# Kernel optimization log

Measured on AMD Instinct MI355X. Metric: run time of the kernel, lower is better.

The kernel has to match this reference:

```python
import jax, jax.numpy as jnp
import numpy as np
from jax import lax

B, CIN, COUT, K, H, W = 16, 256, 256, 3, 128, 128
R = 16  # LoRA rank


def setup_inputs() -> dict:
    key = jax.random.key(0)
    ks = jax.random.split(key, 16)
    s = 0.05
    return {
        "x": jax.random.normal(ks[0], (B, CIN, H, W), jnp.float32),
        "wms": jax.random.normal(ks[1], (2, B, 32), jnp.float32),
        "conv_w": jax.random.normal(ks[2], (COUT, CIN, K, K), jnp.float32) * s,
        "conv_b": jax.random.normal(ks[3], (COUT,), jnp.float32) * s,
        "e1_w1": jax.random.normal(ks[4], (128, 32), jnp.float32) * s,
        "e1_b1": jax.random.normal(ks[5], (128,), jnp.float32) * s,
        "e1_w2": jax.random.normal(ks[6], (256, 128), jnp.float32) * s,
        "e1_b2": jax.random.normal(ks[7], (256,), jnp.float32) * s,
        "e2_w1": jax.random.normal(ks[8], (128, 32), jnp.float32) * s,
        "e2_b1": jax.random.normal(ks[9], (128,), jnp.float32) * s,
        "e2_w2": jax.random.normal(ks[10], (256, 128), jnp.float32) * s,
        "e2_b2": jax.random.normal(ks[11], (256,), jnp.float32) * s,
        "lora_A1": jax.random.normal(ks[12], (R, CIN * K), jnp.float32),
        "lora_A2": jax.random.normal(ks[13], (R, CIN * K), jnp.float32),
        "lora_B": jax.random.normal(ks[14], (COUT * K, R), jnp.float32) * s,
    }


def _embed(v, w1, b1, w2, b2):
    # Linear(32,128) -> LeakyReLU(0.2) -> Linear(128,256)
    h = v @ w1.T + b1
    h = jnp.where(h >= 0, h, 0.2 * h)
    return h @ w2.T + b2


def _conv_same(x, w):
    # NCHW conv, stride 1, padding 1
    return lax.conv_general_dilated(x, w, (1, 1), [(1, 1), (1, 1)],
                                    dimension_numbers=("NCHW", "OIHW", "NCHW"))


def reference(x, wms, conv_w, conv_b, e1_w1, e1_b1, e1_w2, e1_b2,
              e2_w1, e2_b1, e2_w2, e2_b2, lora_A1, lora_A2, lora_B):
    wm1, wm2 = wms[0], wms[1]
    coff1 = _embed(wm1, e1_w1, e1_b1, e1_w2, e1_b2).reshape(B, R, R)
    coff2 = _embed(wm2, e2_w1, e2_b1, e2_w2, e2_b2).reshape(B, R, R)

    org = _conv_same(x, conv_w) + conv_b[None, :, None, None]

    # per-sample LoRA weights: (COUT*K, R) @ (R,R) @ (R, CIN*K) -> (B, COUT, CIN, K, K)
    wA = jnp.einsum('pr,brq,qc->bpc', lora_B, coff1, lora_A1).reshape(B, COUT, CIN, K, K)
    wB = jnp.einsum('pr,brq,qc->bpc', lora_B, coff2, lora_A2).reshape(B, COUT, CIN, K, K)

    def per_sample_conv(xi, wi):
        return _conv_same(xi[None], wi)[0]

    outA = jax.vmap(per_sample_conv)(x, wA)
    outB = jax.vmap(per_sample_conv)(x, wB)
    return org + outA + outB
```

## Files before the change

### kernel.cpp

```cpp
#include <hip/hip_runtime.h>
#include <hip/hip_bf16.h>
#include <stdint.h>

typedef __bf16 bf16x8 __attribute__((ext_vector_type(8)));
typedef float f32x4 __attribute__((ext_vector_type(4)));
typedef unsigned short ushort8v __attribute__((ext_vector_type(8)));

#define NB    16
#define CIN   256
#define COUT  256
#define HH    128
#define WW    128

#define OFF_ZROW  0u
#define OFF_COFF  (1u << 16)
#define OFF_TMPS  (1u << 17)
#define OFF_WEFF  (1u << 20)
#define OFF_XT    (20u * 1024u * 1024u)
#define XT_PER_B  (128u * 128u * 256u * 2u)

__device__ inline void gload16(const void* g, void* l) {
  __builtin_amdgcn_global_load_lds(
      (const __attribute__((address_space(1))) void*)g,
      (__attribute__((address_space(3))) void*)l, 16, 0, 0);
}

__device__ inline ushort f2bf(float f) {
  __hip_bfloat16 h = __float2bfloat16(f);
  union { __hip_bfloat16 b; ushort u; } cv;
  cv.b = h;
  return cv.u;
}

__global__ void k_coff(const float* __restrict__ wms,
                       const float* __restrict__ w1a, const float* __restrict__ b1a,
                       const float* __restrict__ w2a, const float* __restrict__ b2a,
                       const float* __restrict__ w1b, const float* __restrict__ b1b,
                       const float* __restrict__ w2b, const float* __restrict__ b2b,
                       float* __restrict__ coff) {
  int br = blockIdx.x >> 4, b = blockIdx.x & 15;
  const float* w1 = br ? w1b : w1a;
  const float* b1 = br ? b1b : b1a;
  const float* w2 = br ? w2b : w2a;
  const float* b2 = br ? b2b : b2a;
  const float* v = wms + (br * 16 + b) * 32;
  __shared__ float h[128];
  int t = threadIdx.x;
  if (t < 128) {
    float a = b1[t];
#pragma unroll
    for (int i = 0; i < 32; ++i) a += w1[t * 32 + i] * v[i];
    h[t] = a >= 0.f ? a : 0.2f * a;
  }
  __syncthreads();
  float a = b2[t];
  for (int j = 0; j < 128; ++j) a += w2[t * 128 + j] * h[j];
  coff[(br * 16 + b) * 256 + t] = a;
}

__global__ void k_tmps(const float* __restrict__ coff,
                       const float* __restrict__ A1, const float* __restrict__ A2,
                       float* __restrict__ tmpS) {
  int b = blockIdx.x >> 4, r = blockIdx.x & 15;
  __shared__ float c1[16], c2[16];
  int t = threadIdx.x;
  if (t < 16) {
    c1[t] = coff[b * 256 + r * 16 + t];
    c2[t] = coff[(16 + b) * 256 + r * 16 + t];
  }
  __syncthreads();
  for (int c = t; c < 768; c += 256) {
    float s = 0.f;
#pragma unroll
    for (int q = 0; q < 16; ++q) s += c1[q] * A1[q * 768 + c] + c2[q] * A2[q * 768 + c];
    tmpS[(b * 16 + r) * 768 + c] = s;
  }
}

__global__ __launch_bounds__(256) void k_weff(const float* __restrict__ conv_w,
                                              const float* __restrict__ loraB,
                                              const float* __restrict__ tmpS,
                                              __hip_bfloat16* __restrict__ Weff) {
  int bid = blockIdx.x;
  int co = bid & 255, b = bid >> 8;
  int t = threadIdx.x;
  __shared__ float Bs[3][16];
  __shared__ ushort obuf[2304];
  if (t < 48) Bs[t >> 4][t & 15] = loraB[(co * 3 + (t >> 4)) * 16 + (t & 15)];
  __syncthreads();
  const float* T = tmpS + (size_t)b * 16 * 768;
  const float* W = conv_w + (size_t)co * 2304;
#pragma unroll
  for (int k = 0; k < 3; ++k) {
#pragma unroll
    for (int cc = 0; cc < 3; ++cc) {
      int c = cc * 256 + t;
      float s = W[k * 768 + c];
#pragma unroll
      for (int r = 0; r < 16; ++r) s += Bs[k][r] * T[r * 768 + c];
      int f = k * 768 + c;
      int ci = f / 9, tt = f - ci * 9;
      obuf[tt * 256 + ci] = f2bf(s);
    }
  }
  __syncthreads();
#pragma unroll
  for (int tt = 0; tt < 9; ++tt)
    ((ushort*)Weff)[((size_t)(b * 9 + tt) * 256 + co) * 256 + t] = obuf[tt * 256 + t];
}

__global__ __launch_bounds__(256) void k_xt(const float* __restrict__ x,
                                            __hip_bfloat16* __restrict__ xT, int b0) {
  __shared__ ushort t[32][132];
  int bid = blockIdx.x;
  int cb = bid & 7, h = (bid >> 3) & 127, bp = bid >> 10;
  int b = b0 + bp;
  int tid = threadIdx.x;
  int ci2 = tid >> 5, w4 = (tid & 31) * 4;
  const float* srcb = x + ((size_t)(b * 256 + cb * 32) * 128 + h) * 128;
#pragma unroll
  for (int k = 0; k < 4; ++k) {
    int c = ci2 + k * 8;
    float4 v = *(const float4*)(srcb + (size_t)c * 16384 + w4);
    ushort4 u;
    u.x = f2bf(v.x);
    u.y = f2bf(v.y);
    u.z = f2bf(v.z);
    u.w = f2bf(v.w);
    *(ushort4*)&t[c][w4] = u;
  }
  __syncthreads();
  int w = tid >> 1, hf = tid & 1;
  ushort8v o0, o1;
#pragma unroll
  for (int j = 0; j < 8; ++j) {
    o0[j] = t[hf * 16 + j][w];
    o1[j] = t[hf * 16 + 8 + j][w];
  }
  ushort* dst = (ushort*)xT + (size_t)bp * 128 * 128 * 256 +
                ((size_t)h * 128 + w) * 256 + cb * 32 + hf * 16;
  *(ushort8v*)dst = o0;
  *(ushort8v*)(dst + 8) = o1;
}

__global__ __launch_bounds__(256, 2) void k_conv(
    const __hip_bfloat16* __restrict__ xT,
    const __hip_bfloat16* __restrict__ Weff,
    const __hip_bfloat16* __restrict__ zrow,
    const float* __restrict__ cbias,
    float* __restrict__ out, int b0) {
  __shared__ __align__(16) __hip_bfloat16 xs[3 * 130 * 32];
  __shared__ __align__(16) __hip_bfloat16 wbuf[3 * 256 * 32];

  int nwg = gridDim.x;
  int bid0 = blockIdx.x;
  int bid = (bid0 & 7) * (nwg >> 3) + (bid0 >> 3);

  int h0 = bid & 127, bp = bid >> 7;
  int b = b0 + bp;

  int tid = threadIdx.x;
  int wid = tid >> 6, lane = tid & 63;
  int l15 = lane & 15, lh = lane >> 4;
  int wm = wid >> 1;
  int w0 = (wid & 1) * 64;
  int lrow = lane >> 2;
  int sgx = (lane & 3) ^ (((1 + lrow) >> 1) & 3);
  int sgw = (lane & 3) ^ ((lrow >> 1) & 3);
  int asw = (l15 >> 1) & 3;

  if (tid < 192) {
    int ri = tid >> 6, which = (tid >> 5) & 1, ci = tid & 31;
    ((ushort*)xs)[ri * 4160 + (which ? 129 : 0) * 32 + ci] = 0;
  }

  int lha = (lh ^ asw) * 8;
  int a_base = (wm * 128 + l15) * 32 + lha;
  int b_base0 = (w0 + l15 + 0) * 32 + ((lh ^ (((l15 + 0) >> 1) & 3)) * 8);
  int b_base1 = (w0 + l15 + 1) * 32 + ((lh ^ (((l15 + 1) >> 1) & 3)) * 8);
  int b_base2 = (w0 + l15 + 2) * 32 + ((lh ^ (((l15 + 2) >> 1) & 3)) * 8);
  int xoff = lrow * 256 + sgx * 8;
  int woff = lrow * 256 + sgw * 8;

  const __hip_bfloat16* xTb = xT + (size_t)bp * 128 * 128 * 256;
  const __hip_bfloat16* r0 = (h0 > 0)   ? xTb + (size_t)(h0 - 1) * 32768 : zrow;
  const __hip_bfloat16* r1 = xTb + (size_t)h0 * 32768;
  const __hip_bfloat16* r2 = (h0 < 127) ? xTb + (size_t)(h0 + 1) * 32768 : zrow;

  f32x4 acc[8][4];
#pragma unroll
  for (int mf = 0; mf < 8; ++mf)
#pragma unroll
    for (int nf = 0; nf < 4; ++nf) acc[mf][nf] = (f32x4){0.f, 0.f, 0.f, 0.f};

  for (int cb8 = 0; cb8 < 8; ++cb8) {
    int c0 = cb8 * 32;
    __syncthreads();

#pragma unroll
    for (int k = 0; k < 6; ++k) {
      const int ri = k >> 1;
      int wblk = (k & 1) * 4 + wid;
      const __hip_bfloat16* rp = (ri == 0) ? r0 : ((ri == 1) ? r1 : r2);
      gload16((const void*)(rp + wblk * 4096 + c0 + xoff),
              (void*)(xs + ri * 4160 + (1 + wblk * 16) * 32));
    }

#pragma unroll 1
    for (int kh = 0; kh < 3; ++kh) {
      if (kh) __syncthreads();
      const __hip_bfloat16* wtap =
          Weff + ((size_t)(b * 9 + kh * 3) << 16) + c0 + woff;
#pragma unroll
      for (int k = 0; k < 12; ++k) {
        const int kw = k >> 2;
        int cblk = (k & 3) * 4 + wid;
        gload16((const void*)(wtap + kw * 65536 + cblk * 4096),
                (void*)(wbuf + kw * 8192 + cblk * 512));
      }
      __syncthreads();

#pragma unroll
      for (int kw = 0; kw < 3; ++kw) {
        int bb = (kw == 0) ? b_base0 : ((kw == 1) ? b_base1 : b_base2);
        bf16x8 af[8], bfr[4];
#pragma unroll
        for (int mf = 0; mf < 8; ++mf)
          af[mf] = *(const bf16x8*)&wbuf[kw * 8192 + a_base + mf * 512];
#pragma unroll
        for (int nf = 0; nf < 4; ++nf)
          bfr[nf] = *(const bf16x8*)&xs[kh * 4160 + bb + nf * 512];
        __builtin_amdgcn_s_setprio(1);
#pragma unroll
        for (int mf = 0; mf < 8; ++mf)
#pragma unroll
          for (int nf = 0; nf < 4; ++nf)
            acc[mf][nf] = __builtin_amdgcn_mfma_f32_16x16x32_bf16(af[mf], bfr[nf],
                                                                  acc[mf][nf], 0, 0, 0);
        __builtin_amdgcn_s_setprio(0);
      }
    }
  }

#pragma unroll
  for (int mf = 0; mf < 8; ++mf) {
    int cobase = wm * 128 + mf * 16 + lh * 4;
#pragma unroll
    for (int r = 0; r < 4; ++r) {
      int co = cobase + r;
      float bias = cbias[co];
      size_t obase = ((size_t)(b * 256 + co) * 128 + h0) * 128 + w0 + l15;
#pragma unroll
      for (int nf = 0; nf < 4; ++nf) out[obase + nf * 16] = acc[mf][nf][r] + bias;
    }
  }
}

extern "C" void kernel_launch(void* const* d_in, const int* in_sizes, int n_in,
                              void* d_out, int out_size, void* d_ws, size_t ws_size,
                              hipStream_t stream) {
  const float* x      = (const float*)d_in[0];
  const float* wms    = (const float*)d_in[1];
  const float* conv_w = (const float*)d_in[2];
  const float* conv_b = (const float*)d_in[3];
  const float* e1w1   = (const float*)d_in[4];
  const float* e1b1   = (const float*)d_in[5];
  const float* e1w2   = (const float*)d_in[6];
  const float* e1b2   = (const float*)d_in[7];
  const float* e2w1   = (const float*)d_in[8];
  const float* e2b1   = (const float*)d_in[9];
  const float* e2w2   = (const float*)d_in[10];
  const float* e2b2   = (const float*)d_in[11];
  const float* A1     = (const float*)d_in[12];
  const float* A2     = (const float*)d_in[13];
  const float* loraB  = (const float*)d_in[14];
  float* out = (float*)d_out;

  uint8_t* ws = (uint8_t*)d_ws;
  __hip_bfloat16* zrow = (__hip_bfloat16*)(ws + OFF_ZROW);
  float* coff          = (float*)(ws + OFF_COFF);
  float* tmpS          = (float*)(ws + OFF_TMPS);
  __hip_bfloat16* Weff = (__hip_bfloat16*)(ws + OFF_WEFF);
  __hip_bfloat16* xT   = (__hip_bfloat16*)(ws + OFF_XT);

  int G = 16;
  while (G > 1 && (size_t)OFF_XT + (size_t)G * XT_PER_B > ws_size) G >>= 1;

  hipMemsetAsync(zrow, 0, 65536, stream);
  k_coff<<<32, 256, 0, stream>>>(wms, e1w1, e1b1, e1w2, e1b2, e2w1, e2b1, e2w2, e2b2, coff);
  k_tmps<<<256, 256, 0, stream>>>(coff, A1, A2, tmpS);
  k_weff<<<16 * 256, 256, 0, stream>>>(conv_w, loraB, tmpS, Weff);
  for (int g = 0; g < 16; g += G) {
    k_xt<<<G * 1024, 256, 0, stream>>>(x, xT, g);
    k_conv<<<G * 128, 256, 0, stream>>>(xT, Weff, zrow, conv_b, out, g);
  }
}
```

Measured before the change: 446.0 us.

## Load conv weight fragments directly from global into registers with tap prefetch

Drops the LDS weight buffer and its per-kh barriers. Each wave now reads its A-operand weight fragments straight from global memory into registers, and the next tap's fragments are prefetched into a double buffer while the current tap's MFMAs run. The intent is to remove LDS staging traffic and two of the three barrier stages per input-channel block, and to overlap weight loads with compute. The cost is more VGPR pressure from two fragment arrays, uncoalesced or repeated global/L2 weight reads across waves and blocks, and a hand-tuned vmcnt wait that assumes a fixed load ordering.

```diff
diff --git a/kernel.cpp b/kernel.cpp
--- a/kernel.cpp
+++ b/kernel.cpp
@@ -150,7 +150,6 @@
     const float* __restrict__ cbias,
     float* __restrict__ out, int b0) {
   __shared__ __align__(16) __hip_bfloat16 xs[3 * 130 * 32];
-  __shared__ __align__(16) __hip_bfloat16 wbuf[3 * 256 * 32];
 
   int nwg = gridDim.x;
   int bid0 = blockIdx.x;
@@ -166,26 +165,23 @@
   int w0 = (wid & 1) * 64;
   int lrow = lane >> 2;
   int sgx = (lane & 3) ^ (((1 + lrow) >> 1) & 3);
-  int sgw = (lane & 3) ^ ((lrow >> 1) & 3);
-  int asw = (l15 >> 1) & 3;
 
   if (tid < 192) {
     int ri = tid >> 6, which = (tid >> 5) & 1, ci = tid & 31;
     ((ushort*)xs)[ri * 4160 + (which ? 129 : 0) * 32 + ci] = 0;
   }
 
-  int lha = (lh ^ asw) * 8;
-  int a_base = (wm * 128 + l15) * 32 + lha;
+  int a_off = (wm * 128 + l15) * 256 + lh * 8;
   int b_base0 = (w0 + l15 + 0) * 32 + ((lh ^ (((l15 + 0) >> 1) & 3)) * 8);
   int b_base1 = (w0 + l15 + 1) * 32 + ((lh ^ (((l15 + 1) >> 1) & 3)) * 8);
   int b_base2 = (w0 + l15 + 2) * 32 + ((lh ^ (((l15 + 2) >> 1) & 3)) * 8);
   int xoff = lrow * 256 + sgx * 8;
-  int woff = lrow * 256 + sgw * 8;
 
   const __hip_bfloat16* xTb = xT + (size_t)bp * 128 * 128 * 256;
   const __hip_bfloat16* r0 = (h0 > 0)   ? xTb + (size_t)(h0 - 1) * 32768 : zrow;
   const __hip_bfloat16* r1 = xTb + (size_t)h0 * 32768;
   const __hip_bfloat16* r2 = (h0 < 127) ? xTb + (size_t)(h0 + 1) * 32768 : zrow;
+  const __hip_bfloat16* wbase = Weff + ((size_t)(b * 9) << 16);
 
   f32x4 acc[8][4];
 #pragma unroll
@@ -193,9 +189,37 @@
 #pragma unroll
     for (int nf = 0; nf < 4; ++nf) acc[mf][nf] = (f32x4){0.f, 0.f, 0.f, 0.f};
 
+  __syncthreads();
+
+  bf16x8 aA[8], aB[8];
+
+#define CONV_TAP(CUR, NXT, TT, KH, KW, PREF)                                   \
+  {                                                                            \
+    if (PREF) {                                                                \
+      const __hip_bfloat16* an = wb + (((TT) + 1) << 16);                      \
+      _Pragma("unroll")                                                        \
+      for (int mf = 0; mf < 8; ++mf)                                           \
+        NXT[mf] = *(const bf16x8*)(an + mf * 4096);                            \
+    }                                                                          \
+    const int bb = (KW == 0) ? b_base0 : ((KW == 1) ? b_base1 : b_base2);      \
+    bf16x8 bfr[4];                                                             \
+    _Pragma("unroll")                                                          \
+    for (int nf = 0; nf < 4; ++nf)                                             \
+      bfr[nf] = *(const bf16x8*)&xs[(KH) * 4160 + bb + nf * 512];              \
+    __builtin_amdgcn_s_setprio(1);                                             \
+    _Pragma("unroll")                                                          \
+    for (int mf = 0; mf < 8; ++mf)                                             \
+      _Pragma("unroll")                                                        \
+      for (int nf = 0; nf < 4; ++nf)                                           \
+        acc[mf][nf] = __builtin_amdgcn_mfma_f32_16x16x32_bf16(                 \
+            CUR[mf], bfr[nf], acc[mf][nf], 0, 0, 0);                           \
+    __builtin_amdgcn_s_setprio(0);                                             \
+  }
+
+#pragma unroll 1
   for (int cb8 = 0; cb8 < 8; ++cb8) {
     int c0 = cb8 * 32;
-    __syncthreads();
+    __builtin_amdgcn_s_barrier();
 
 #pragma unroll
     for (int k = 0; k < 6; ++k) {
@@ -206,41 +230,24 @@
               (void*)(xs + ri * 4160 + (1 + wblk * 16) * 32));
     }
 
-#pragma unroll 1
-    for (int kh = 0; kh < 3; ++kh) {
-      if (kh) __syncthreads();
-      const __hip_bfloat16* wtap =
-          Weff + ((size_t)(b * 9 + kh * 3) << 16) + c0 + woff;
-#pragma unroll
-      for (int k = 0; k < 12; ++k) {
-        const int kw = k >> 2;
-        int cblk = (k & 3) * 4 + wid;
-        gload16((const void*)(wtap + kw * 65536 + cblk * 4096),
-                (void*)(wbuf + kw * 8192 + cblk * 512));
-      }
-      __syncthreads();
-
-#pragma unroll
-      for (int kw = 0; kw < 3; ++kw) {
-        int bb = (kw == 0) ? b_base0 : ((kw == 1) ? b_base1 : b_base2);
-        bf16x8 af[8], bfr[4];
-#pragma unroll
-        for (int mf = 0; mf < 8; ++mf)
-          af[mf] = *(const bf16x8*)&wbuf[kw * 8192 + a_base + mf * 512];
-#pragma unroll
-        for (int nf = 0; nf < 4; ++nf)
-          bfr[nf] = *(const bf16x8*)&xs[kh * 4160 + bb + nf * 512];
-        __builtin_amdgcn_s_setprio(1);
-#pragma unroll
-        for (int mf = 0; mf < 8; ++mf)
-#pragma unroll
-          for (int nf = 0; nf < 4; ++nf)
-            acc[mf][nf] = __builtin_amdgcn_mfma_f32_16x16x32_bf16(af[mf], bfr[nf],
-                                                                  acc[mf][nf], 0, 0, 0);
-        __builtin_amdgcn_s_setprio(0);
-      }
-    }
-  }
+    const __hip_bfloat16* wb = wbase + c0 + a_off;
+#pragma unroll
+    for (int mf = 0; mf < 8; ++mf) aA[mf] = *(const bf16x8*)(wb + mf * 4096);
+
+    asm volatile("s_waitcnt vmcnt(8)" ::: "memory");
+    __builtin_amdgcn_s_barrier();
+
+    CONV_TAP(aA, aB, 0, 0, 0, 1);
+    CONV_TAP(aB, aA, 1, 0, 1, 1);
+    CONV_TAP(aA, aB, 2, 0, 2, 1);
+    CONV_TAP(aB, aA, 3, 1, 0, 1);
+    CONV_TAP(aA, aB, 4, 1, 1, 1);
+    CONV_TAP(aB, aA, 5, 1, 2, 1);
+    CONV_TAP(aA, aB, 6, 2, 0, 1);
+    CONV_TAP(aB, aA, 7, 2, 1, 1);
+    CONV_TAP(aA, aB, 8, 2, 2, 0);
+  }
+#undef CONV_TAP
 
 #pragma unroll
   for (int mf = 0; mf < 8; ++mf) {
```

New measurement: 705.1 us. +58.1%, slower.
